# Kernel tuning notes

Measured on AMD Instinct MI355X. Metric: run time of the kernel, lower is better.

Reference implementation:

```python
import jax, jax.numpy as jnp
import numpy as np

B, T, C = 4, 2048, 1024
H = 16
D = C // H  # head_dim = 64


def setup_inputs() -> dict:
    key = jax.random.key(0)
    ks = jax.random.split(key, 11)
    s = 0.02
    return {
        "q": jax.random.normal(ks[0], (B, T, C), jnp.float32),
        "k": jax.random.normal(ks[1], (B, T, C), jnp.float32),
        "v": jax.random.normal(ks[2], (B, T, C), jnp.float32),
        "Wq": jax.random.normal(ks[3], (C, C), jnp.float32) * s,
        "bq": jnp.zeros((C,), jnp.float32),
        "Wk": jax.random.normal(ks[4], (C, C), jnp.float32) * s,
        "bk": jnp.zeros((C,), jnp.float32),
        "Wv": jax.random.normal(ks[5], (C, C), jnp.float32) * s,
        "bv": jnp.zeros((C,), jnp.float32),
        "Wo": jax.random.normal(ks[6], (C, C), jnp.float32) * s,
        "bo": jnp.zeros((C,), jnp.float32),
    }


def reference(q, k, v, Wq, bq, Wk, bk, Wv, bv, Wo, bo):
    # projections (torch Linear: x @ W.T + b)
    qh = (q @ Wq.T + bq).reshape(B, T, H, D).transpose(0, 2, 1, 3)  # [B,H,T,D]
    kh = (k @ Wk.T + bk).reshape(B, T, H, D).transpose(0, 2, 1, 3)
    vh = (v @ Wv.T + bv).reshape(B, T, H, D).transpose(0, 2, 1, 3)
    scores = jnp.einsum('bhqd,bhkd->bhqk', qh, kh) * (D ** -0.5)  # [B,H,T,T]
    # causal mask (is_causal=True)
    causal = jnp.tril(jnp.ones((T, T), bool))
    scores = jnp.where(causal, scores, -jnp.inf)
    probs = jax.nn.softmax(scores, axis=-1)
    # dropout_rate=0.0 -> identity in eval mode
    out = jnp.einsum('bhqk,bhkd->bhqd', probs, vh)  # [B,H,T,D]
    out = out.transpose(0, 2, 1, 3).reshape(B, T, C)
    return out @ Wo.T + bo
```

## Files before the change

kernel.cpp:

```cpp
#include <hip/hip_runtime.h>
#include <hip/hip_bf16.h>

typedef __attribute__((ext_vector_type(8))) short bf16x8;
typedef __attribute__((ext_vector_type(4))) float f32x4;
typedef __attribute__((ext_vector_type(16))) float f32x16;

__device__ __forceinline__ unsigned short f2bf(float x) {
  union { float f; unsigned u; } v; v.f = x;
  unsigned r = v.u + 0x7fffu + ((v.u >> 16) & 1u);
  return (unsigned short)(r >> 16);
}

__device__ __forceinline__ unsigned cvtpk_bf16(float lo, float hi) {
  unsigned r;
  asm("v_cvt_pk_bf16_f32 %0, %1, %2" : "=v"(r) : "v"(lo), "v"(hi));
  return r;
}
__device__ __forceinline__ void pl32swap(unsigned &a, unsigned &b) {
  asm volatile("v_permlane32_swap_b32 %0, %1" : "+v"(a), "+v"(b));
}

__device__ __forceinline__ void gload_lds16(const void* g, void* l) {
  __builtin_amdgcn_global_load_lds((const __attribute__((address_space(1))) void*)g,
                                   (__attribute__((address_space(3))) void*)l, 16, 0, 0);
}

#define SWZ(x) ((x) ^ ((((x) >> 7) & 7) << 4))

__global__ __launch_bounds__(256) void proj_gemm3(
    const float* __restrict__ A0, const float* __restrict__ A1, const float* __restrict__ A2,
    const float* __restrict__ W0, const float* __restrict__ W1, const float* __restrict__ W2,
    const float* __restrict__ b0, const float* __restrict__ b1, const float* __restrict__ b2,
    unsigned short* __restrict__ o0, unsigned short* __restrict__ o1, unsigned short* __restrict__ o2) {
  const int K = 1024;
  __shared__ __align__(16) unsigned short As[2][128][40];
  __shared__ __align__(16) unsigned short Bs[2][128][40];
  const int z = blockIdx.z;
  const float* A = (z == 0) ? A0 : (z == 1) ? A1 : A2;
  const float* W = (z == 0) ? W0 : (z == 1) ? W1 : W2;
  const float* bias = (z == 0) ? b0 : (z == 1) ? b1 : b2;
  unsigned short* out = (z == 0) ? o0 : (z == 1) ? o1 : o2;
  const float scale = (z == 0) ? 0.125f * 1.4426950408889634f : 1.0f;
  const int vtrans = (z == 2);

  const int tid = threadIdx.x;
  const int row0 = blockIdx.x * 128;
  const int col0 = blockIdx.y * 128;
  const int lane = tid & 63;
  const int wave = tid >> 6;
  const int wm = (wave >> 1) * 64, wn = (wave & 1) * 64;
  const int fr = lane & 15;
  const int fk = (lane >> 4) * 8;

  f32x4 acc[4][4] = {};

  const int srow = tid >> 1;
  const int sc0 = (tid & 1) << 4;

  auto stage = [&](int buf, int kt) {
    const int k0 = kt * 32;
    {
      const float4* ap = (const float4*)(&A[(size_t)(row0 + srow) * K + k0 + sc0]);
      float4 x0 = ap[0], x1 = ap[1], x2 = ap[2], x3 = ap[3];
      uint4 u, v;
      u.x = cvtpk_bf16(x0.x, x0.y); u.y = cvtpk_bf16(x0.z, x0.w);
      u.z = cvtpk_bf16(x1.x, x1.y); u.w = cvtpk_bf16(x1.z, x1.w);
      v.x = cvtpk_bf16(x2.x, x2.y); v.y = cvtpk_bf16(x2.z, x2.w);
      v.z = cvtpk_bf16(x3.x, x3.y); v.w = cvtpk_bf16(x3.z, x3.w);
      *(uint4*)(&As[buf][srow][sc0]) = u;
      *(uint4*)(&As[buf][srow][sc0 + 8]) = v;
    }
    {
      const float4* bp = (const float4*)(&W[(size_t)(col0 + srow) * K + k0 + sc0]);
      float4 x0 = bp[0], x1 = bp[1], x2 = bp[2], x3 = bp[3];
      uint4 u, v;
      u.x = cvtpk_bf16(x0.x, x0.y); u.y = cvtpk_bf16(x0.z, x0.w);
      u.z = cvtpk_bf16(x1.x, x1.y); u.w = cvtpk_bf16(x1.z, x1.w);
      v.x = cvtpk_bf16(x2.x, x2.y); v.y = cvtpk_bf16(x2.z, x2.w);
      v.z = cvtpk_bf16(x3.x, x3.y); v.w = cvtpk_bf16(x3.z, x3.w);
      *(uint4*)(&Bs[buf][srow][sc0]) = u;
      *(uint4*)(&Bs[buf][srow][sc0 + 8]) = v;
    }
  };

  stage(0, 0);
  __syncthreads();
  const int NK = K / 32;
  for (int kt = 0; kt < NK; ++kt) {
    const int buf = kt & 1;
    if (kt + 1 < NK) stage(buf ^ 1, kt + 1);
    bf16x8 af[4], bfv[4];
#pragma unroll
    for (int i = 0; i < 4; ++i) {
      af[i] = *(const bf16x8*)(&As[buf][wm + i * 16 + fr][fk]);
      bfv[i] = *(const bf16x8*)(&Bs[buf][wn + i * 16 + fr][fk]);
    }
#pragma unroll
    for (int i = 0; i < 4; ++i)
#pragma unroll
      for (int j = 0; j < 4; ++j)
        acc[i][j] = __builtin_amdgcn_mfma_f32_16x16x32_bf16(af[i], bfv[j], acc[i][j], 0, 0, 0);
    __syncthreads();
  }

#pragma unroll
  for (int j = 0; j < 4; ++j) {
    const int n = col0 + wn + j * 16 + fr;
    const float bv = bias[n];
    const int h = n >> 6, d = n & 63;
#pragma unroll
    for (int i = 0; i < 4; ++i) {
      const int mrow = row0 + wm + i * 16 + (lane >> 4) * 4;
#pragma unroll
      for (int r = 0; r < 4; ++r) {
        const int m = mrow + r;
        const int b = m >> 11, t = m & 2047;
        const float val = (acc[i][j][r] + bv) * scale;
        if (vtrans)
          out[(((size_t)b * 16 + h) * 64 + d) * 2048 + t] = f2bf(val);
        else
          out[(((size_t)b * 16 + h) * 2048 + t) * 64 + d] = f2bf(val);
      }
    }
  }
}

__global__ __launch_bounds__(256) void out_gemm(
    const unsigned short* __restrict__ A, const float* __restrict__ W,
    const float* __restrict__ bias, float* __restrict__ out) {
  const int K = 1024;
  __shared__ __align__(16) unsigned short As[2][128][40];
  __shared__ __align__(16) unsigned short Bs[2][128][40];
  const int tid = threadIdx.x;
  const int row0 = blockIdx.x * 128;
  const int col0 = blockIdx.y * 128;
  const int lane = tid & 63;
  const int wave = tid >> 6;
  const int wm = (wave >> 1) * 64, wn = (wave & 1) * 64;
  const int fr = lane & 15;
  const int fk = (lane >> 4) * 8;

  f32x4 acc[4][4] = {};

  const int srow = tid >> 1;
  const int sc0 = (tid & 1) << 4;

  auto stage = [&](int buf, int kt) {
    const int k0 = kt * 32;
    {
      const uint4* ap = (const uint4*)(&A[(size_t)(row0 + srow) * K + k0 + sc0]);
      uint4 ra = ap[0], rb = ap[1];
      *(uint4*)(&As[buf][srow][sc0]) = ra;
      *(uint4*)(&As[buf][srow][sc0 + 8]) = rb;
    }
    {
      const float4* bp = (const float4*)(&W[(size_t)(col0 + srow) * K + k0 + sc0]);
      float4 x0 = bp[0], x1 = bp[1], x2 = bp[2], x3 = bp[3];
      uint4 u, v;
      u.x = cvtpk_bf16(x0.x, x0.y); u.y = cvtpk_bf16(x0.z, x0.w);
      u.z = cvtpk_bf16(x1.x, x1.y); u.w = cvtpk_bf16(x1.z, x1.w);
      v.x = cvtpk_bf16(x2.x, x2.y); v.y = cvtpk_bf16(x2.z, x2.w);
      v.z = cvtpk_bf16(x3.x, x3.y); v.w = cvtpk_bf16(x3.z, x3.w);
      *(uint4*)(&Bs[buf][srow][sc0]) = u;
      *(uint4*)(&Bs[buf][srow][sc0 + 8]) = v;
    }
  };

  stage(0, 0);
  __syncthreads();
  const int NK = K / 32;
  for (int kt = 0; kt < NK; ++kt) {
    const int buf = kt & 1;
    if (kt + 1 < NK) stage(buf ^ 1, kt + 1);
    bf16x8 af[4], bfv[4];
#pragma unroll
    for (int i = 0; i < 4; ++i) {
      af[i] = *(const bf16x8*)(&As[buf][wm + i * 16 + fr][fk]);
      bfv[i] = *(const bf16x8*)(&Bs[buf][wn + i * 16 + fr][fk]);
    }
#pragma unroll
    for (int i = 0; i < 4; ++i)
#pragma unroll
      for (int j = 0; j < 4; ++j)
        acc[i][j] = __builtin_amdgcn_mfma_f32_16x16x32_bf16(af[i], bfv[j], acc[i][j], 0, 0, 0);
    __syncthreads();
  }

#pragma unroll
  for (int j = 0; j < 4; ++j) {
    const int n = col0 + wn + j * 16 + fr;
    const float bv = bias[n];
#pragma unroll
    for (int i = 0; i < 4; ++i) {
      const int mrow = row0 + wm + i * 16 + (lane >> 4) * 4;
#pragma unroll
      for (int r = 0; r < 4; ++r) {
        const int m = mrow + r;
        out[(size_t)m * 1024 + n] = acc[i][j][r] + bv;
      }
    }
  }
}

__global__ __launch_bounds__(256) void attn_mfma(
    const unsigned short* __restrict__ qh, const unsigned short* __restrict__ kh,
    const unsigned short* __restrict__ vT, unsigned short* __restrict__ Ob) {
  __shared__ __align__(16) unsigned short Klds[2][64 * 64];
  __shared__ __align__(16) unsigned short Vlds[2][64 * 64];

  const int tid = threadIdx.x;
  const int lane = tid & 63;
  const int w = tid >> 6;
  const int bh = blockIdx.y;
  const int b = bh >> 4, h = bh & 15;
  const int q32 = lane & 31;
  const int hi = lane >> 5;

  const char* kbase = (const char*)(kh + (size_t)bh * 2048 * 64);
  const char* vbase = (const char*)(vT + (size_t)bh * 64 * 2048);

  const int lrow = lane >> 3;
  const int cb = (((lane & 7) ^ lrow) << 4);

  auto stage = [&](int buf, int t) {
    const int kv0 = t * 64;
#pragma unroll
    for (int j = 0; j < 2; ++j) {
      const int c = w * 2 + j;
      const int r = c * 8 + lrow;
      gload_lds16(kbase + (size_t)(kv0 + r) * 128 + cb,
                  (char*)Klds[buf] + c * 1024);
      gload_lds16(vbase + (size_t)r * 4096 + (size_t)kv0 * 2 + cb,
                  (char*)Vlds[buf] + c * 1024);
    }
  };

  for (int pass = 0; pass < 2; ++pass) {
    const int qt = pass == 0 ? (15 - (int)blockIdx.x) : (int)blockIdx.x;
    const int qb = qt * 128 + w * 32;
    const int nt = 2 * qt + 2;

    bf16x8 qf[4];
    {
      const unsigned short* qp = qh + ((size_t)bh * 2048 + qb + q32) * 64;
#pragma unroll
      for (int kk = 0; kk < 4; ++kk)
        qf[kk] = *(const bf16x8*)(qp + kk * 16 + hi * 8);
    }

    f32x16 acc_o[2] = {};
    float m_run = -INFINITY, l_run = 0.f;

    stage(0, 0);
    __syncthreads();

    int cur = 0;
    for (int t = 0; t < nt; ++t) {
      const int kv0 = t * 64;
      if (t + 1 < nt) stage(cur ^ 1, t + 1);

      if (kv0 < qb + 32) {
        const char* Kb = (const char*)Klds[cur];
        const char* Vb = (const char*)Vlds[cur];

        f32x16 sacc[2] = {};
        __builtin_amdgcn_s_setprio(1);
#pragma unroll
        for (int kk = 0; kk < 4; ++kk) {
          bf16x8 kf0 = *(const bf16x8*)(Kb + SWZ((q32) * 128 + kk * 32 + hi * 16));
          bf16x8 kf1 = *(const bf16x8*)(Kb + SWZ((32 + q32) * 128 + kk * 32 + hi * 16));
          sacc[0] = __builtin_amdgcn_mfma_f32_32x32x16_bf16(kf0, qf[kk], sacc[0], 0, 0, 0);
          sacc[1] = __builtin_amdgcn_mfma_f32_32x32x16_bf16(kf1, qf[kk], sacc[1], 0, 0, 0);
        }
        __builtin_amdgcn_s_setprio(0);

        if (kv0 + 64 > qb) {
          const int qa = qb + q32;
#pragma unroll
          for (int mkv = 0; mkv < 2; ++mkv)
#pragma unroll
            for (int r = 0; r < 16; ++r) {
              const int kva = kv0 + mkv * 32 + 4 * hi + (r & 3) + 8 * (r >> 2);
              if (kva > qa) sacc[mkv][r] = -INFINITY;
            }
        }

        float mx = -INFINITY;
#pragma unroll
        for (int mkv = 0; mkv < 2; ++mkv)
#pragma unroll
          for (int r = 0; r < 16; ++r) mx = fmaxf(mx, sacc[mkv][r]);
        mx = fmaxf(mx, __shfl_xor(mx, 32));
        if (!__all(mx <= m_run + 8.f)) {
          const float mnew = fmaxf(m_run, mx);
          const float al = exp2f(m_run - mnew);
          m_run = mnew;
          l_run *= al;
          acc_o[0] = acc_o[0] * al;
          acc_o[1] = acc_o[1] * al;
        }

        float ls = 0.f;
        unsigned W[2][8];
#pragma unroll
        for (int mkv = 0; mkv < 2; ++mkv)
#pragma unroll
          for (int s = 0; s < 8; ++s) {
            const float p0 = exp2f(sacc[mkv][2 * s] - m_run);
            const float p1 = exp2f(sacc[mkv][2 * s + 1] - m_run);
            ls += p0 + p1;
            W[mkv][s] = cvtpk_bf16(p0, p1);
          }
        ls += __shfl_xor(ls, 32);
        l_run += ls;

#pragma unroll
        for (int mkv = 0; mkv < 2; ++mkv) {
          pl32swap(W[mkv][0], W[mkv][2]);
          pl32swap(W[mkv][1], W[mkv][3]);
          pl32swap(W[mkv][4], W[mkv][6]);
          pl32swap(W[mkv][5], W[mkv][7]);
        }

        __builtin_amdgcn_s_setprio(1);
#pragma unroll
        for (int wg = 0; wg < 4; ++wg) {
          union { unsigned u[4]; bf16x8 v; } pk;
          pk.u[0] = W[wg >> 1][(wg & 1) * 4 + 0];
          pk.u[1] = W[wg >> 1][(wg & 1) * 4 + 1];
          pk.u[2] = W[wg >> 1][(wg & 1) * 4 + 2];
          pk.u[3] = W[wg >> 1][(wg & 1) * 4 + 3];
          bf16x8 vf0 = *(const bf16x8*)(Vb + SWZ((q32) * 128 + wg * 32 + hi * 16));
          bf16x8 vf1 = *(const bf16x8*)(Vb + SWZ((32 + q32) * 128 + wg * 32 + hi * 16));
          acc_o[0] = __builtin_amdgcn_mfma_f32_32x32x16_bf16(vf0, pk.v, acc_o[0], 0, 0, 0);
          acc_o[1] = __builtin_amdgcn_mfma_f32_32x32x16_bf16(vf1, pk.v, acc_o[1], 0, 0, 0);
        }
        __builtin_amdgcn_s_setprio(0);
      }

      __syncthreads();
      cur ^= 1;
    }

    {
      const float inv = 1.0f / l_run;
      const int qa = qb + q32;
      unsigned short* op = Ob + ((size_t)b * 2048 + qa) * 1024 + h * 64;
#pragma unroll
      for (int md = 0; md < 2; ++md)
#pragma unroll
        for (int rr = 0; rr < 4; ++rr) {
          uint2 u;
          u.x = cvtpk_bf16(acc_o[md][rr * 4 + 0] * inv, acc_o[md][rr * 4 + 1] * inv);
          u.y = cvtpk_bf16(acc_o[md][rr * 4 + 2] * inv, acc_o[md][rr * 4 + 3] * inv);
          *(uint2*)(op + md * 32 + rr * 8 + hi * 4) = u;
        }
    }
  }
}

extern "C" void kernel_launch(void* const* d_in, const int* in_sizes, int n_in,
                              void* d_out, int out_size, void* d_ws, size_t ws_size,
                              hipStream_t stream) {
  (void)in_sizes; (void)n_in; (void)out_size; (void)ws_size;
  const float* q = (const float*)d_in[0];
  const float* k = (const float*)d_in[1];
  const float* v = (const float*)d_in[2];
  const float* Wq = (const float*)d_in[3];
  const float* bq = (const float*)d_in[4];
  const float* Wk = (const float*)d_in[5];
  const float* bk = (const float*)d_in[6];
  const float* Wv = (const float*)d_in[7];
  const float* bv = (const float*)d_in[8];
  const float* Wo = (const float*)d_in[9];
  const float* bo = (const float*)d_in[10];
  float* out = (float*)d_out;

  const size_t SZ = (size_t)4 * 16 * 2048 * 64;
  unsigned short* qh = (unsigned short*)d_ws;
  unsigned short* kh = qh + SZ;
  unsigned short* vT = kh + SZ;
  unsigned short* Ob = vT + SZ;

  dim3 g1(64, 8, 3), b1(256);
  proj_gemm3<<<g1, b1, 0, stream>>>(q, k, v, Wq, Wk, Wv, bq, bk, bv, qh, kh, vT);

  dim3 g2(8, 64), b2(256);
  attn_mfma<<<g2, b2, 0, stream>>>(qh, kh, vT, Ob);

  dim3 g3(64, 8), b3(256);
  out_gemm<<<g3, b3, 0, stream>>>(Ob, Wo, bo, out);
}
```

Baseline: 246.1 us.

## Pre-convert weights to bf16 and stage GEMM tiles via direct global-to-LDS loads

Adds a kernel that converts all four weight matrices to bf16 once per call, folding the softmax scale into Wq. The projection and output GEMMs then load the bf16 tiles straight into a swizzled LDS layout with global_load_lds instead of converting fp32 in registers. The fp32 A-operand loads in the projection are issued before the MFMAs and stored to LDS after them, to overlap latency, and the V-transposed epilogue uses packed vector stores. This costs an extra launch and extra workspace, and the swizzle mapping has to be exactly right.

```diff
diff --git a/kernel.cpp b/kernel.cpp
--- a/kernel.cpp
+++ b/kernel.cpp
@@ -27,156 +27,199 @@
 
 #define SWZ(x) ((x) ^ ((((x) >> 7) & 7) << 4))
 
+__global__ __launch_bounds__(256) void cvt_w(
+    const float* __restrict__ W0, const float* __restrict__ W1,
+    const float* __restrict__ W2, const float* __restrict__ W3,
+    unsigned short* __restrict__ o0, unsigned short* __restrict__ o1,
+    unsigned short* __restrict__ o2, unsigned short* __restrict__ o3,
+    float s0) {
+  const int z = blockIdx.y;
+  const float* W = (z == 0) ? W0 : (z == 1) ? W1 : (z == 2) ? W2 : W3;
+  unsigned short* o = (z == 0) ? o0 : (z == 1) ? o1 : (z == 2) ? o2 : o3;
+  const float s = (z == 0) ? s0 : 1.0f;
+  const int i = blockIdx.x * 256 + threadIdx.x;
+  const float4 x = ((const float4*)W)[i];
+  uint2 u;
+  u.x = cvtpk_bf16(x.x * s, x.y * s);
+  u.y = cvtpk_bf16(x.z * s, x.w * s);
+  ((uint2*)o)[i] = u;
+}
+
+
 __global__ __launch_bounds__(256) void proj_gemm3(
     const float* __restrict__ A0, const float* __restrict__ A1, const float* __restrict__ A2,
-    const float* __restrict__ W0, const float* __restrict__ W1, const float* __restrict__ W2,
+    const unsigned short* __restrict__ W0b, const unsigned short* __restrict__ W1b,
+    const unsigned short* __restrict__ W2b,
     const float* __restrict__ b0, const float* __restrict__ b1, const float* __restrict__ b2,
-    unsigned short* __restrict__ o0, unsigned short* __restrict__ o1, unsigned short* __restrict__ o2) {
+    unsigned short* __restrict__ o0, unsigned short* __restrict__ o1,
+    unsigned short* __restrict__ o2) {
   const int K = 1024;
-  __shared__ __align__(16) unsigned short As[2][128][40];
-  __shared__ __align__(16) unsigned short Bs[2][128][40];
+  __shared__ __align__(16) unsigned short As[2][4096];
+  __shared__ __align__(16) unsigned short Bs[2][4096];
   const int z = blockIdx.z;
   const float* A = (z == 0) ? A0 : (z == 1) ? A1 : A2;
-  const float* W = (z == 0) ? W0 : (z == 1) ? W1 : W2;
+  const unsigned short* Wb = (z == 0) ? W0b : (z == 1) ? W1b : W2b;
   const float* bias = (z == 0) ? b0 : (z == 1) ? b1 : b2;
   unsigned short* out = (z == 0) ? o0 : (z == 1) ? o1 : o2;
-  const float scale = (z == 0) ? 0.125f * 1.4426950408889634f : 1.0f;
+  const float bscale = (z == 0) ? 0.125f * 1.4426950408889634f : 1.0f;
   const int vtrans = (z == 2);
 
   const int tid = threadIdx.x;
   const int row0 = blockIdx.x * 128;
   const int col0 = blockIdx.y * 128;
   const int lane = tid & 63;
-  const int wave = tid >> 6;
-  const int wm = (wave >> 1) * 64, wn = (wave & 1) * 64;
+  const int w = tid >> 6;
+  const int wm = (w >> 1) * 64, wn = (w & 1) * 64;
   const int fr = lane & 15;
-  const int fk = (lane >> 4) * 8;
+  const int g = lane >> 4;
+  const int frh = fr >> 1;
+  const int gcf = ((fr & 1) * 4 + g) ^ frh;
+  const int aoff = wm * 64 + frh * 128 + gcf * 16;
+  const int boff = wn * 64 + frh * 128 + gcf * 16;
+
+  const int ar = tid >> 2;
+  const int acq = tid & 3;
+  const float* asrc0 = &A[(size_t)(row0 + ar) * K + acq * 8];
+  const float* asrc1 = asrc0 + (size_t)64 * K;
+  const int awr = (ar >> 1) * 128 + ((((ar & 1) * 4 + acq) ^ ((ar >> 1) & 7)) * 16);
+
+  const unsigned short* bsrc[2];
+  int bldso[2];
+#pragma unroll
+  for (int j = 0; j < 2; ++j) {
+    const int L = (w * 2 + j) * 64 + lane;
+    const int pp = L >> 3, gc = L & 7;
+    const int e = gc ^ (pp & 7);
+    const int r = pp * 2 + (e >> 2), c = e & 3;
+    bsrc[j] = Wb + (size_t)(col0 + r) * K + c * 8;
+    bldso[j] = (w * 2 + j) * 1024;
+  }
 
   f32x4 acc[4][4] = {};
-
-  const int srow = tid >> 1;
-  const int sc0 = (tid & 1) << 4;
-
-  auto stage = [&](int buf, int kt) {
-    const int k0 = kt * 32;
-    {
-      const float4* ap = (const float4*)(&A[(size_t)(row0 + srow) * K + k0 + sc0]);
-      float4 x0 = ap[0], x1 = ap[1], x2 = ap[2], x3 = ap[3];
-      uint4 u, v;
-      u.x = cvtpk_bf16(x0.x, x0.y); u.y = cvtpk_bf16(x0.z, x0.w);
-      u.z = cvtpk_bf16(x1.x, x1.y); u.w = cvtpk_bf16(x1.z, x1.w);
-      v.x = cvtpk_bf16(x2.x, x2.y); v.y = cvtpk_bf16(x2.z, x2.w);
-      v.z = cvtpk_bf16(x3.x, x3.y); v.w = cvtpk_bf16(x3.z, x3.w);
-      *(uint4*)(&As[buf][srow][sc0]) = u;
-      *(uint4*)(&As[buf][srow][sc0 + 8]) = v;
-    }
-    {
-      const float4* bp = (const float4*)(&W[(size_t)(col0 + srow) * K + k0 + sc0]);
-      float4 x0 = bp[0], x1 = bp[1], x2 = bp[2], x3 = bp[3];
-      uint4 u, v;
-      u.x = cvtpk_bf16(x0.x, x0.y); u.y = cvtpk_bf16(x0.z, x0.w);
-      u.z = cvtpk_bf16(x1.x, x1.y); u.w = cvtpk_bf16(x1.z, x1.w);
-      v.x = cvtpk_bf16(x2.x, x2.y); v.y = cvtpk_bf16(x2.z, x2.w);
-      v.z = cvtpk_bf16(x3.x, x3.y); v.w = cvtpk_bf16(x3.z, x3.w);
-      *(uint4*)(&Bs[buf][srow][sc0]) = u;
-      *(uint4*)(&Bs[buf][srow][sc0 + 8]) = v;
-    }
+  float4 la[4];
+
+  auto loadA = [&](int kt) {
+    const float* s0 = asrc0 + kt * 32;
+    const float* s1 = asrc1 + kt * 32;
+    la[0] = *(const float4*)s0; la[1] = *(const float4*)(s0 + 4);
+    la[2] = *(const float4*)s1; la[3] = *(const float4*)(s1 + 4);
   };
-
-  stage(0, 0);
+  auto storeA = [&](int buf) {
+    uint4 u0, u1;
+    u0.x = cvtpk_bf16(la[0].x, la[0].y); u0.y = cvtpk_bf16(la[0].z, la[0].w);
+    u0.z = cvtpk_bf16(la[1].x, la[1].y); u0.w = cvtpk_bf16(la[1].z, la[1].w);
+    u1.x = cvtpk_bf16(la[2].x, la[2].y); u1.y = cvtpk_bf16(la[2].z, la[2].w);
+    u1.z = cvtpk_bf16(la[3].x, la[3].y); u1.w = cvtpk_bf16(la[3].z, la[3].w);
+    char* base = (char*)As[buf];
+    *(uint4*)(base + awr) = u0;
+    *(uint4*)(base + awr + 4096) = u1;
+  };
+  auto stageB = [&](int buf, int kt) {
+#pragma unroll
+    for (int j = 0; j < 2; ++j)
+      gload_lds16(bsrc[j] + kt * 32, (char*)Bs[buf] + bldso[j]);
+  };
+
+  loadA(0); stageB(0, 0); storeA(0);
   __syncthreads();
-  const int NK = K / 32;
-  for (int kt = 0; kt < NK; ++kt) {
+  for (int kt = 0; kt < 32; ++kt) {
     const int buf = kt & 1;
-    if (kt + 1 < NK) stage(buf ^ 1, kt + 1);
+    if (kt < 31) { loadA(kt + 1); stageB(buf ^ 1, kt + 1); }
+    const char* Ab = (const char*)As[buf];
+    const char* Bb = (const char*)Bs[buf];
     bf16x8 af[4], bfv[4];
 #pragma unroll
     for (int i = 0; i < 4; ++i) {
-      af[i] = *(const bf16x8*)(&As[buf][wm + i * 16 + fr][fk]);
-      bfv[i] = *(const bf16x8*)(&Bs[buf][wn + i * 16 + fr][fk]);
+      af[i] = *(const bf16x8*)(Ab + aoff + i * 1024);
+      bfv[i] = *(const bf16x8*)(Bb + boff + i * 1024);
     }
 #pragma unroll
     for (int i = 0; i < 4; ++i)
 #pragma unroll
       for (int j = 0; j < 4; ++j)
         acc[i][j] = __builtin_amdgcn_mfma_f32_16x16x32_bf16(af[i], bfv[j], acc[i][j], 0, 0, 0);
+    if (kt < 31) storeA(buf ^ 1);
     __syncthreads();
   }
 
 #pragma unroll
   for (int j = 0; j < 4; ++j) {
     const int n = col0 + wn + j * 16 + fr;
-    const float bv = bias[n];
+    const float bv = bias[n] * bscale;
     const int h = n >> 6, d = n & 63;
 #pragma unroll
     for (int i = 0; i < 4; ++i) {
-      const int mrow = row0 + wm + i * 16 + (lane >> 4) * 4;
-#pragma unroll
-      for (int r = 0; r < 4; ++r) {
-        const int m = mrow + r;
-        const int b = m >> 11, t = m & 2047;
-        const float val = (acc[i][j][r] + bv) * scale;
-        if (vtrans)
-          out[(((size_t)b * 16 + h) * 64 + d) * 2048 + t] = f2bf(val);
-        else
-          out[(((size_t)b * 16 + h) * 2048 + t) * 64 + d] = f2bf(val);
+      const int mrow = row0 + wm + i * 16 + g * 4;
+      const int b = mrow >> 11, t0 = mrow & 2047;
+      if (vtrans) {
+        uint2 u;
+        u.x = cvtpk_bf16(acc[i][j][0] + bv, acc[i][j][1] + bv);
+        u.y = cvtpk_bf16(acc[i][j][2] + bv, acc[i][j][3] + bv);
+        *(uint2*)(&out[(((size_t)b * 16 + h) * 64 + d) * 2048 + t0]) = u;
+      } else {
+#pragma unroll
+        for (int r = 0; r < 4; ++r)
+          out[(((size_t)b * 16 + h) * 2048 + (t0 + r)) * 64 + d] = f2bf(acc[i][j][r] + bv);
       }
     }
   }
 }
 
 __global__ __launch_bounds__(256) void out_gemm(
-    const unsigned short* __restrict__ A, const float* __restrict__ W,
+    const unsigned short* __restrict__ A, const unsigned short* __restrict__ Wb,
     const float* __restrict__ bias, float* __restrict__ out) {
   const int K = 1024;
-  __shared__ __align__(16) unsigned short As[2][128][40];
-  __shared__ __align__(16) unsigned short Bs[2][128][40];
+  __shared__ __align__(16) unsigned short As[2][4096];
+  __shared__ __align__(16) unsigned short Bs[2][4096];
   const int tid = threadIdx.x;
   const int row0 = blockIdx.x * 128;
   const int col0 = blockIdx.y * 128;
   const int lane = tid & 63;
-  const int wave = tid >> 6;
-  const int wm = (wave >> 1) * 64, wn = (wave & 1) * 64;
+  const int w = tid >> 6;
+  const int wm = (w >> 1) * 64, wn = (w & 1) * 64;
   const int fr = lane & 15;
-  const int fk = (lane >> 4) * 8;
+  const int g = lane >> 4;
+  const int frh = fr >> 1;
+  const int gcf = ((fr & 1) * 4 + g) ^ frh;
+  const int aoff = wm * 64 + frh * 128 + gcf * 16;
+  const int boff = wn * 64 + frh * 128 + gcf * 16;
+
+  const unsigned short* asrc[2];
+  const unsigned short* bsrc[2];
+  int ldso[2];
+#pragma unroll
+  for (int j = 0; j < 2; ++j) {
+    const int L = (w * 2 + j) * 64 + lane;
+    const int pp = L >> 3, gc = L & 7;
+    const int e = gc ^ (pp & 7);
+    const int r = pp * 2 + (e >> 2), c = e & 3;
+    asrc[j] = A + (size_t)(row0 + r) * K + c * 8;
+    bsrc[j] = Wb + (size_t)(col0 + r) * K + c * 8;
+    ldso[j] = (w * 2 + j) * 1024;
+  }
 
   f32x4 acc[4][4] = {};
 
-  const int srow = tid >> 1;
-  const int sc0 = (tid & 1) << 4;
-
   auto stage = [&](int buf, int kt) {
-    const int k0 = kt * 32;
-    {
-      const uint4* ap = (const uint4*)(&A[(size_t)(row0 + srow) * K + k0 + sc0]);
-      uint4 ra = ap[0], rb = ap[1];
-      *(uint4*)(&As[buf][srow][sc0]) = ra;
-      *(uint4*)(&As[buf][srow][sc0 + 8]) = rb;
-    }
-    {
-      const float4* bp = (const float4*)(&W[(size_t)(col0 + srow) * K + k0 + sc0]);
-      float4 x0 = bp[0], x1 = bp[1], x2 = bp[2], x3 = bp[3];
-      uint4 u, v;
-      u.x = cvtpk_bf16(x0.x, x0.y); u.y = cvtpk_bf16(x0.z, x0.w);
-      u.z = cvtpk_bf16(x1.x, x1.y); u.w = cvtpk_bf16(x1.z, x1.w);
-      v.x = cvtpk_bf16(x2.x, x2.y); v.y = cvtpk_bf16(x2.z, x2.w);
-      v.z = cvtpk_bf16(x3.x, x3.y); v.w = cvtpk_bf16(x3.z, x3.w);
-      *(uint4*)(&Bs[buf][srow][sc0]) = u;
-      *(uint4*)(&Bs[buf][srow][sc0 + 8]) = v;
+#pragma unroll
+    for (int j = 0; j < 2; ++j) {
+      gload_lds16(asrc[j] + kt * 32, (char*)As[buf] + ldso[j]);
+      gload_lds16(bsrc[j] + kt * 32, (char*)Bs[buf] + ldso[j]);
     }
   };
 
   stage(0, 0);
   __syncthreads();
-  const int NK = K / 32;
-  for (int kt = 0; kt < NK; ++kt) {
+  for (int kt = 0; kt < 32; ++kt) {
     const int buf = kt & 1;
-    if (kt + 1 < NK) stage(buf ^ 1, kt + 1);
+    if (kt < 31) stage(buf ^ 1, kt + 1);
+    const char* Ab = (const char*)As[buf];
+    const char* Bb = (const char*)Bs[buf];
     bf16x8 af[4], bfv[4];
 #pragma unroll
     for (int i = 0; i < 4; ++i) {
-      af[i] = *(const bf16x8*)(&As[buf][wm + i * 16 + fr][fk]);
-      bfv[i] = *(const bf16x8*)(&Bs[buf][wn + i * 16 + fr][fk]);
+      af[i] = *(const bf16x8*)(Ab + aoff + i * 1024);
+      bfv[i] = *(const bf16x8*)(Bb + boff + i * 1024);
     }
 #pragma unroll
     for (int i = 0; i < 4; ++i)
@@ -192,12 +235,10 @@
     const float bv = bias[n];
 #pragma unroll
     for (int i = 0; i < 4; ++i) {
-      const int mrow = row0 + wm + i * 16 + (lane >> 4) * 4;
-#pragma unroll
-      for (int r = 0; r < 4; ++r) {
-        const int m = mrow + r;
-        out[(size_t)m * 1024 + n] = acc[i][j][r] + bv;
-      }
+      const int mrow = row0 + wm + i * 16 + g * 4;
+#pragma unroll
+      for (int r = 0; r < 4; ++r)
+        out[(size_t)(mrow + r) * 1024 + n] = acc[i][j][r] + bv;
     }
   }
 }
@@ -377,17 +418,26 @@
   float* out = (float*)d_out;
 
   const size_t SZ = (size_t)4 * 16 * 2048 * 64;
+  const size_t WSZ = (size_t)1024 * 1024;
   unsigned short* qh = (unsigned short*)d_ws;
   unsigned short* kh = qh + SZ;
   unsigned short* vT = kh + SZ;
   unsigned short* Ob = vT + SZ;
+  unsigned short* Wqb = Ob + SZ;
+  unsigned short* Wkb = Wqb + WSZ;
+  unsigned short* Wvb = Wkb + WSZ;
+  unsigned short* Wob = Wvb + WSZ;
+
+  dim3 g0(1024, 4), b0(256);
+  cvt_w<<<g0, b0, 0, stream>>>(Wq, Wk, Wv, Wo, Wqb, Wkb, Wvb, Wob,
+                               0.125f * 1.4426950408889634f);
 
   dim3 g1(64, 8, 3), b1(256);
-  proj_gemm3<<<g1, b1, 0, stream>>>(q, k, v, Wq, Wk, Wv, bq, bk, bv, qh, kh, vT);
+  proj_gemm3<<<g1, b1, 0, stream>>>(q, k, v, Wqb, Wkb, Wvb, bq, bk, bv, qh, kh, vT);
 
   dim3 g2(8, 64), b2(256);
   attn_mfma<<<g2, b2, 0, stream>>>(qh, kh, vT, Ob);
 
   dim3 g3(64, 8), b3(256);
-  out_gemm<<<g3, b3, 0, stream>>>(Ob, Wo, bo, out);
-}
+  out_gemm<<<g3, b3, 0, stream>>>(Ob, Wob, bo, out);
+}
```

Result: faster. 223.7 us (-9.1%).
